# Optimization experiments

Measured on AMD Instinct MI355X. Metric: run time of the kernel, lower is better.

Reference implementation:

```python
import jax, jax.numpy as jnp
import numpy as np

E = 262144      # n_edges
T = 2097152     # n_triplets
F = 128         # embed_size
A = 64          # angle_int_embed_size
RBF = 6         # num_radial
SBF = 42        # num_spherical * num_radial
B = 8           # basis_int_embed_size
NB = 1          # residual layers before skip
NA = 2          # residual layers after skip


def _rn(k, shape):
    # fan-in scaled init like default Linear init
    return jax.random.normal(k, shape, jnp.float32) / np.sqrt(shape[-2])


def setup_inputs() -> dict:
    key = jax.random.key(0)
    ks = jax.random.split(key, 18)
    return dict(
        m_input=jax.random.normal(ks[0], (E, F), jnp.float32),
        rbf=jax.random.normal(ks[1], (E, RBF), jnp.float32),
        sbf=jax.random.normal(ks[2], (T, SBF), jnp.float32),
        reduce_to_ji=jax.random.randint(ks[3], (T,), 0, E),
        expand_to_kj=jax.random.randint(ks[4], (T,), 0, E),
        W_kj=_rn(ks[5], (F, F)), b_kj=jnp.zeros((F,), jnp.float32),
        W_rbf1=_rn(ks[6], (RBF, B)), W_rbf2=_rn(ks[7], (B, F)),
        W_sbf1=_rn(ks[8], (SBF, B)), W_sbf2=_rn(ks[9], (B, A)),
        W_down=_rn(ks[10], (F, A)), W_up=_rn(ks[11], (A, F)),
        W_ji=_rn(ks[12], (F, F)), b_ji=jnp.zeros((F,), jnp.float32),
        W_res_before=_rn(ks[13], (NB, 2, F, F)),
        b_res_before=jnp.zeros((NB, 2, F), jnp.float32),
        W_final=_rn(ks[14], (F, F)), b_final=jnp.zeros((F,), jnp.float32),
        W_res_after=_rn(ks[15], (NA, 2, F, F)),
        b_res_after=jnp.zeros((NA, 2, F), jnp.float32),
    )


def _residual(x, W, b):
    # W: [2, F, F], b: [2, F]; two swish-activated linears + skip
    h = jax.nn.swish(x @ W[0] + b[0])
    h = jax.nn.swish(h @ W[1] + b[1])
    return x + h


def reference(m_input, rbf, sbf, reduce_to_ji, expand_to_kj,
              W_kj, b_kj, W_rbf1, W_rbf2, W_sbf1, W_sbf2,
              W_down, W_up, W_ji, b_ji,
              W_res_before, b_res_before, W_final, b_final,
              W_res_after, b_res_after):
    # dense_kj branch, modulated by projected RBF
    m_ang = jax.nn.swish(m_input @ W_kj + b_kj)          # [E, F]
    rbf_p = (rbf @ W_rbf1) @ W_rbf2                      # [E, F]
    m_ang = m_ang * rbf_p
    m_ang = jax.nn.swish(m_ang @ W_down)                 # [E, A]
    # expand edges -> triplets, modulate with projected SBF
    m_kj = m_ang[expand_to_kj]                           # [T, A]
    sbf_p = (sbf @ W_sbf1) @ W_sbf2                      # [T, A]
    m_kj = m_kj * sbf_p
    # scatter-reduce triplets back to edges (high precision fp32 segment sum)
    agg = jax.ops.segment_sum(m_kj.astype(jnp.float32), reduce_to_ji,
                              num_segments=E)            # [E, A]
    prop = jax.nn.swish(agg @ W_up)                      # [E, F]
    m_ji = jax.nn.swish(m_input @ W_ji + b_ji)           # [E, F]
    m = m_ji + prop
    for i in range(NB):
        m = _residual(m, W_res_before[i], b_res_before[i])
    m = jax.nn.swish(m @ W_final + b_final)
    m = m + m_input
    for i in range(NA):
        m = _residual(m, W_res_after[i], b_res_after[i])
    return m
```

## Files before the change

kernel.cpp:

```cpp
#include <hip/hip_runtime.h>

#define EN 262144
#define TN 2097152
#define CAP 32
#define OFCAP 262144

__device__ __forceinline__ float swishf(float x){ return x/(1.f+__expf(-x)); }

template<int K, int NC, class AF, class EP>
__device__ __forceinline__ void gemm_stage(const float* __restrict__ Wg, AF af, EP ep)
{
  constexpr int CPT = NC/16;
  const int tc = threadIdx.x & 15;
  const int te = threadIdx.x >> 4;
  const int c0 = tc*CPT;
  float acc[4][CPT];
#pragma unroll
  for(int i=0;i<4;i++)
#pragma unroll
    for(int j=0;j<CPT;j++) acc[i][j]=0.f;

  for (int k=0;k<K;k+=4){
    float a[4][4];
#pragma unroll
    for(int i=0;i<4;i++){
      float4 t = af(te*4+i, k);
      a[i][0]=t.x; a[i][1]=t.y; a[i][2]=t.z; a[i][3]=t.w;
    }
#pragma unroll
    for(int kk=0;kk<4;kk++){
      float w[CPT];
      const float* wp = Wg + (size_t)(k+kk)*NC + c0;
      float4 w0 = *(const float4*)wp;
      w[0]=w0.x; w[1]=w0.y; w[2]=w0.z; w[3]=w0.w;
      if constexpr (CPT==8){
        float4 w1 = *(const float4*)(wp+4);
        w[4]=w1.x; w[5]=w1.y; w[6]=w1.z; w[7]=w1.w;
      }
#pragma unroll
      for(int i=0;i<4;i++)
#pragma unroll
        for(int j=0;j<CPT;j++)
          acc[i][j] = fmaf(a[i][kk], w[j], acc[i][j]);
    }
  }
  ep(acc, te, c0);
}

__global__ void k0_prebasis(const float* __restrict__ Ws1, const float* __restrict__ Ws2,
                            const float* __restrict__ Wr1, const float* __restrict__ Wr2,
                            float* __restrict__ Psbf, float* __restrict__ Prbf)
{
  int idx = blockIdx.x*256 + threadIdx.x;
  if (idx < 42*64){
    int r = idx>>6, a = idx&63;
    float s=0.f;
#pragma unroll
    for(int j=0;j<8;j++) s = fmaf(Ws1[r*8+j], Ws2[j*64+a], s);
    Psbf[idx]=s;
  }
  if (idx < 6*128){
    int r = idx>>7, c = idx&127;
    float s=0.f;
#pragma unroll
    for(int j=0;j<8;j++) s = fmaf(Wr1[r*8+j], Wr2[j*128+c], s);
    Prbf[idx]=s;
  }
}

__global__ __launch_bounds__(256) void k1_pre(
  const float* __restrict__ mi, const float* __restrict__ rbf,
  const float* __restrict__ Wkj, const float* __restrict__ bkj,
  const float* __restrict__ Wdown, const float* __restrict__ Prbf,
  float* __restrict__ mang2)
{
  __shared__ __align__(16) float hs[64*128];
  const int eb = blockIdx.x*64;

  auto afG = [&](int e,int k)->float4{
    return *(const float4*)(mi + (size_t)(eb+e)*128 + k);
  };
  gemm_stage<128,128>(Wkj, afG, [&](float (&acc)[4][8], int te, int c0){
    float bb[8];
#pragma unroll
    for(int j=0;j<8;j++) bb[j]=bkj[c0+j];
#pragma unroll
    for(int i=0;i<4;i++){
      int e = te*4+i;
      size_t ge = (size_t)(eb+e);
      float rp[8];
#pragma unroll
      for(int j=0;j<8;j++) rp[j]=0.f;
#pragma unroll
      for(int r=0;r<6;r++){
        float rv = rbf[ge*6+r];
        const float* prow = Prbf + r*128 + c0;
        float4 p0 = *(const float4*)prow;
        float4 p1 = *(const float4*)(prow+4);
        rp[0]=fmaf(rv,p0.x,rp[0]); rp[1]=fmaf(rv,p0.y,rp[1]);
        rp[2]=fmaf(rv,p0.z,rp[2]); rp[3]=fmaf(rv,p0.w,rp[3]);
        rp[4]=fmaf(rv,p1.x,rp[4]); rp[5]=fmaf(rv,p1.y,rp[5]);
        rp[6]=fmaf(rv,p1.z,rp[6]); rp[7]=fmaf(rv,p1.w,rp[7]);
      }
#pragma unroll
      for(int j=0;j<8;j++)
        hs[e*128+c0+j] = swishf(acc[i][j]+bb[j])*rp[j];
    }
  });
  __syncthreads();
  auto afL = [&](int e,int k)->float4{ return *(const float4*)(hs + e*128 + k); };
  gemm_stage<128,64>(Wdown, afL, [&](float (&acc)[4][4], int te, int c0){
#pragma unroll
    for(int i=0;i<4;i++){
      size_t ge = (size_t)(eb + te*4+i);
      float4 v = make_float4(swishf(acc[i][0]),swishf(acc[i][1]),
                             swishf(acc[i][2]),swishf(acc[i][3]));
      *(float4*)(mang2 + ge*64 + c0) = v;
    }
  });
}

__global__ __launch_bounds__(256) void ka_bin(
  const int* __restrict__ rji,
  int* __restrict__ cnt, int* __restrict__ perm,
  int* __restrict__ ofcnt, int* __restrict__ oflist)
{
  size_t t = (size_t)blockIdx.x*256 + threadIdx.x;
  int ji = rji[t];
  int slot = atomicAdd(cnt + ji, 1);
  if (slot < CAP) {
    perm[(size_t)ji*CAP + slot] = (int)t;
  } else {
    int o = atomicAdd(ofcnt, 1);
    if (o < OFCAP) oflist[o] = (int)t;
  }
}

__global__ __launch_bounds__(256) void k2_gather(
  const float* __restrict__ sbf, const int* __restrict__ ekj,
  const int* __restrict__ cnt, const int* __restrict__ perm,
  const float* __restrict__ Psbf, const float* __restrict__ mang2,
  float* __restrict__ agg)
{
  const int lane = threadIdx.x & 63;
  const int wid  = blockIdx.x*4 + (threadIdx.x >> 6);
  const int nw   = gridDim.x*4;

  float P[42];
#pragma unroll
  for (int r=0;r<42;r++) P[r] = Psbf[r*64 + lane];

  for (int e = wid; e < EN; e += nw) {
    int n = cnt[e]; if (n > CAP) n = CAP;
    const int* pl = perm + (size_t)e*CAP;
    float acc = 0.f;
    for (int i=0;i<n;i++) {
      int t  = __builtin_amdgcn_readfirstlane(pl[i]);
      int kj = __builtin_amdgcn_readfirstlane(ekj[t]);
      float mv = mang2[(size_t)kj*64 + lane];
      const float* su = sbf + (size_t)t*42;
      float sp0 = 0.f, sp1 = 0.f;
#pragma unroll
      for (int r=0;r<42;r+=2){
        sp0 = fmaf(su[r],   P[r],   sp0);
        sp1 = fmaf(su[r+1], P[r+1], sp1);
      }
      acc = fmaf(mv, sp0 + sp1, acc);
    }
    agg[(size_t)e*64 + lane] = acc;
  }
}

__global__ __launch_bounds__(256) void kof(
  const int* __restrict__ ofcnt, const int* __restrict__ oflist,
  const float* __restrict__ sbf, const int* __restrict__ rji,
  const int* __restrict__ ekj, const float* __restrict__ Psbf,
  const float* __restrict__ mang2, float* __restrict__ agg)
{
  int n = *ofcnt; if (n > OFCAP) n = OFCAP;
  const int lane = threadIdx.x & 63;
  for (int i = blockIdx.x*4 + (threadIdx.x>>6); i < n; i += gridDim.x*4) {
    int t = oflist[i];
    const float* su = sbf + (size_t)t*42;
    float sp = 0.f;
#pragma unroll
    for (int r=0;r<42;r++) sp = fmaf(su[r], Psbf[r*64+lane], sp);
    float val = mang2[(size_t)ekj[t]*64 + lane] * sp;
    atomicAdd(agg + (size_t)rji[t]*64 + lane, val);
  }
}

__global__ __launch_bounds__(256) void k3_post(
  const float* __restrict__ mi, const float* __restrict__ agg,
  const float* __restrict__ Wup, const float* __restrict__ Wji, const float* __restrict__ bji,
  const float* __restrict__ Wrb, const float* __restrict__ brb,
  const float* __restrict__ Wfin, const float* __restrict__ bfin,
  const float* __restrict__ Wra, const float* __restrict__ bra,
  float* __restrict__ outp)
{
  __shared__ __align__(16) float xs[64*128];
  __shared__ __align__(16) float hs[64*128];
  const int eb = blockIdx.x*64;

  auto afA = [&](int e,int k)->float4{ return *(const float4*)(agg + (size_t)(eb+e)*64 + k); };
  auto afG = [&](int e,int k)->float4{ return *(const float4*)(mi + (size_t)(eb+e)*128 + k); };
  auto afX = [&](int e,int k)->float4{ return *(const float4*)(xs + e*128 + k); };
  auto afH = [&](int e,int k)->float4{ return *(const float4*)(hs + e*128 + k); };

  gemm_stage<64,128>(Wup, afA, [&](float (&acc)[4][8], int te, int c0){
#pragma unroll
    for(int i=0;i<4;i++){ int e=te*4+i;
#pragma unroll
      for(int j=0;j<8;j++) xs[e*128+c0+j] = swishf(acc[i][j]);
    }
  });
  gemm_stage<128,128>(Wji, afG, [&](float (&acc)[4][8], int te, int c0){
    float bb[8];
#pragma unroll
    for(int j=0;j<8;j++) bb[j]=bji[c0+j];
#pragma unroll
    for(int i=0;i<4;i++){ int e=te*4+i;
#pragma unroll
      for(int j=0;j<8;j++) xs[e*128+c0+j] += swishf(acc[i][j]+bb[j]);
    }
  });
  __syncthreads();
  gemm_stage<128,128>(Wrb, afX, [&](float (&acc)[4][8], int te, int c0){
    float bb[8];
#pragma unroll
    for(int j=0;j<8;j++) bb[j]=brb[c0+j];
#pragma unroll
    for(int i=0;i<4;i++){ int e=te*4+i;
#pragma unroll
      for(int j=0;j<8;j++) hs[e*128+c0+j] = swishf(acc[i][j]+bb[j]);
    }
  });
  __syncthreads();
  gemm_stage<128,128>(Wrb+16384, afH, [&](float (&acc)[4][8], int te, int c0){
    float bb[8];
#pragma unroll
    for(int j=0;j<8;j++) bb[j]=brb[128+c0+j];
#pragma unroll
    for(int i=0;i<4;i++){ int e=te*4+i;
#pragma unroll
      for(int j=0;j<8;j++) xs[e*128+c0+j] += swishf(acc[i][j]+bb[j]);
    }
  });
  __syncthreads();
  gemm_stage<128,128>(Wfin, afX, [&](float (&acc)[4][8], int te, int c0){
    float bb[8];
#pragma unroll
    for(int j=0;j<8;j++) bb[j]=bfin[c0+j];
#pragma unroll
    for(int i=0;i<4;i++){ int e=te*4+i;
      const float* p = mi + (size_t)(eb+e)*128 + c0;
      float4 m0 = *(const float4*)p;
      float4 m1 = *(const float4*)(p+4);
      float m[8] = {m0.x,m0.y,m0.z,m0.w,m1.x,m1.y,m1.z,m1.w};
#pragma unroll
      for(int j=0;j<8;j++) hs[e*128+c0+j] = swishf(acc[i][j]+bb[j]) + m[j];
    }
  });
  __syncthreads();
  gemm_stage<128,128>(Wra, afH, [&](float (&acc)[4][8], int te, int c0){
    float bb[8];
#pragma unroll
    for(int j=0;j<8;j++) bb[j]=bra[c0+j];
#pragma unroll
    for(int i=0;i<4;i++){ int e=te*4+i;
#pragma unroll
      for(int j=0;j<8;j++) xs[e*128+c0+j] = swishf(acc[i][j]+bb[j]);
    }
  });
  __syncthreads();
  gemm_stage<128,128>(Wra+16384, afX, [&](float (&acc)[4][8], int te, int c0){
    float bb[8];
#pragma unroll
    for(int j=0;j<8;j++) bb[j]=bra[128+c0+j];
#pragma unroll
    for(int i=0;i<4;i++){ int e=te*4+i;
#pragma unroll
      for(int j=0;j<8;j++) hs[e*128+c0+j] += swishf(acc[i][j]+bb[j]);
    }
  });
  __syncthreads();
  gemm_stage<128,128>(Wra+32768, afH, [&](float (&acc)[4][8], int te, int c0){
    float bb[8];
#pragma unroll
    for(int j=0;j<8;j++) bb[j]=bra[256+c0+j];
#pragma unroll
    for(int i=0;i<4;i++){ int e=te*4+i;
#pragma unroll
      for(int j=0;j<8;j++) xs[e*128+c0+j] = swishf(acc[i][j]+bb[j]);
    }
  });
  __syncthreads();
  gemm_stage<128,128>(Wra+49152, afX, [&](float (&acc)[4][8], int te, int c0){
    float bb[8];
#pragma unroll
    for(int j=0;j<8;j++) bb[j]=bra[384+c0+j];
#pragma unroll
    for(int i=0;i<4;i++){ int e=te*4+i;
      size_t ge = (size_t)(eb+e);
      float o[8];
#pragma unroll
      for(int j=0;j<8;j++) o[j] = hs[e*128+c0+j] + swishf(acc[i][j]+bb[j]);
      *(float4*)(outp + ge*128 + c0)   = make_float4(o[0],o[1],o[2],o[3]);
      *(float4*)(outp + ge*128 + c0+4) = make_float4(o[4],o[5],o[6],o[7]);
    }
  });
}

extern "C" void kernel_launch(void* const* d_in, const int* in_sizes, int n_in,
                              void* d_out, int out_size, void* d_ws, size_t ws_size,
                              hipStream_t stream)
{
  (void)in_sizes; (void)n_in; (void)out_size; (void)ws_size;
  const float* mi   = (const float*)d_in[0];
  const float* rbf  = (const float*)d_in[1];
  const float* sbf  = (const float*)d_in[2];
  const int*   rji  = (const int*)d_in[3];
  const int*   ekj  = (const int*)d_in[4];
  const float* Wkj  = (const float*)d_in[5];
  const float* bkj  = (const float*)d_in[6];
  const float* Wr1  = (const float*)d_in[7];
  const float* Wr2  = (const float*)d_in[8];
  const float* Ws1  = (const float*)d_in[9];
  const float* Ws2  = (const float*)d_in[10];
  const float* Wdn  = (const float*)d_in[11];
  const float* Wup  = (const float*)d_in[12];
  const float* Wji  = (const float*)d_in[13];
  const float* bji  = (const float*)d_in[14];
  const float* Wrb  = (const float*)d_in[15];
  const float* brb  = (const float*)d_in[16];
  const float* Wfin = (const float*)d_in[17];
  const float* bfin = (const float*)d_in[18];
  const float* Wra  = (const float*)d_in[19];
  const float* bra  = (const float*)d_in[20];

  char* ws = (char*)d_ws;
  float* mang2 = (float*)ws;
  float* agg   = (float*)(ws + (size_t)EN*64*4);
  float* Psbf  = (float*)(ws + (size_t)EN*64*8);
  float* Prbf  = Psbf + 42*64;
  int*   cnt   = (int*)(ws + (size_t)EN*64*8 + 65536);
  int*   ofcnt = cnt + EN;
  int*   perm  = (int*)((char*)cnt + (size_t)EN*4 + 256);
  int*   oflist= perm + (size_t)EN*CAP;

  hipMemsetAsync(cnt, 0, (size_t)EN*4 + 256, stream);
  k0_prebasis<<<11, 256, 0, stream>>>(Ws1, Ws2, Wr1, Wr2, Psbf, Prbf);
  ka_bin<<<TN/256, 256, 0, stream>>>(rji, cnt, perm, ofcnt, oflist);
  k1_pre<<<EN/64, 256, 0, stream>>>(mi, rbf, Wkj, bkj, Wdn, Prbf, mang2);
  k2_gather<<<2048, 256, 0, stream>>>(sbf, ekj, cnt, perm, Psbf, mang2, agg);
  kof<<<64, 256, 0, stream>>>(ofcnt, oflist, sbf, rji, ekj, Psbf, mang2, agg);
  k3_post<<<EN/64, 256, 0, stream>>>(mi, agg, Wup, Wji, bji, Wrb, brb,
                                     Wfin, bfin, Wra, bra, (float*)d_out);
}
```

Measured before the change: 2.763 ms.

## Keep residual stream in registers, single padded LDS tile, prefetch gather indices

The post-processing kernel now holds the residual stream (x, h) in registers and uses a single padded LDS buffer (stride 132) for GEMM operand staging. This halves shared memory per block, and launch bounds request 4 blocks per SM for more occupancy. LDS writes are vectorized and padded to reduce bank conflicts in both k1 and k3. The gather kernel loads up to 32 triplet and kj indices per edge in one wave-wide read, broadcasts them with shuffles and prefetches the next mang2 row. The extra syncs and higher register pressure may limit the occupancy gain.

```diff
diff --git a/kernel.cpp b/kernel.cpp
--- a/kernel.cpp
+++ b/kernel.cpp
@@ -4,17 +4,18 @@
 #define TN 2097152
 #define CAP 32
 #define OFCAP 262144
+#define LDP 132
 
 __device__ __forceinline__ float swishf(float x){ return x/(1.f+__expf(-x)); }
 
-template<int K, int NC, class AF, class EP>
-__device__ __forceinline__ void gemm_stage(const float* __restrict__ Wg, AF af, EP ep)
+template<int K, int NC, class AF>
+__device__ __forceinline__ void gemm_core(const float* __restrict__ Wg, AF af,
+                                          float (&acc)[4][NC/16])
 {
   constexpr int CPT = NC/16;
   const int tc = threadIdx.x & 15;
   const int te = threadIdx.x >> 4;
   const int c0 = tc*CPT;
-  float acc[4][CPT];
 #pragma unroll
   for(int i=0;i<4;i++)
 #pragma unroll
@@ -44,7 +45,6 @@
           acc[i][j] = fmaf(a[i][kk], w[j], acc[i][j]);
     }
   }
-  ep(acc, te, c0);
 }
 
 __global__ void k0_prebasis(const float* __restrict__ Ws1, const float* __restrict__ Ws2,
@@ -74,13 +74,18 @@
   const float* __restrict__ Wdown, const float* __restrict__ Prbf,
   float* __restrict__ mang2)
 {
-  __shared__ __align__(16) float hs[64*128];
+  __shared__ __align__(16) float hs[64*LDP];
   const int eb = blockIdx.x*64;
+  const int tc = threadIdx.x & 15;
+  const int te = threadIdx.x >> 4;
 
   auto afG = [&](int e,int k)->float4{
     return *(const float4*)(mi + (size_t)(eb+e)*128 + k);
   };
-  gemm_stage<128,128>(Wkj, afG, [&](float (&acc)[4][8], int te, int c0){
+  float acc[4][8];
+  gemm_core<128,128>(Wkj, afG, acc);
+  {
+    const int c0 = tc*8;
     float bb[8];
 #pragma unroll
     for(int j=0;j<8;j++) bb[j]=bkj[c0+j];
@@ -102,22 +107,28 @@
         rp[4]=fmaf(rv,p1.x,rp[4]); rp[5]=fmaf(rv,p1.y,rp[5]);
         rp[6]=fmaf(rv,p1.z,rp[6]); rp[7]=fmaf(rv,p1.w,rp[7]);
       }
-#pragma unroll
-      for(int j=0;j<8;j++)
-        hs[e*128+c0+j] = swishf(acc[i][j]+bb[j])*rp[j];
-    }
-  });
+      float o[8];
+#pragma unroll
+      for(int j=0;j<8;j++) o[j] = swishf(acc[i][j]+bb[j])*rp[j];
+      float* p = hs + e*LDP + c0;
+      *(float4*)p     = make_float4(o[0],o[1],o[2],o[3]);
+      *(float4*)(p+4) = make_float4(o[4],o[5],o[6],o[7]);
+    }
+  }
   __syncthreads();
-  auto afL = [&](int e,int k)->float4{ return *(const float4*)(hs + e*128 + k); };
-  gemm_stage<128,64>(Wdown, afL, [&](float (&acc)[4][4], int te, int c0){
+  auto afL = [&](int e,int k)->float4{ return *(const float4*)(hs + e*LDP + k); };
+  float acc2[4][4];
+  gemm_core<128,64>(Wdown, afL, acc2);
+  {
+    const int c0 = tc*4;
 #pragma unroll
     for(int i=0;i<4;i++){
       size_t ge = (size_t)(eb + te*4+i);
-      float4 v = make_float4(swishf(acc[i][0]),swishf(acc[i][1]),
-                             swishf(acc[i][2]),swishf(acc[i][3]));
+      float4 v = make_float4(swishf(acc2[i][0]),swishf(acc2[i][1]),
+                             swishf(acc2[i][2]),swishf(acc2[i][3]));
       *(float4*)(mang2 + ge*64 + c0) = v;
     }
-  });
+  }
 }
 
 __global__ __launch_bounds__(256) void ka_bin(
@@ -153,19 +164,32 @@
   for (int e = wid; e < EN; e += nw) {
     int n = cnt[e]; if (n > CAP) n = CAP;
     const int* pl = perm + (size_t)e*CAP;
+    int tv  = (lane < n) ? pl[lane] : 0;
+    int kjv = (lane < n) ? ekj[tv]  : 0;
+
     float acc = 0.f;
+    int tcur = 0; float mvcur = 0.f;
+    if (n > 0) {
+      tcur = __builtin_amdgcn_readfirstlane(__shfl(tv, 0));
+      int kj0 = __builtin_amdgcn_readfirstlane(__shfl(kjv, 0));
+      mvcur = mang2[(size_t)kj0*64 + lane];
+    }
     for (int i=0;i<n;i++) {
-      int t  = __builtin_amdgcn_readfirstlane(pl[i]);
-      int kj = __builtin_amdgcn_readfirstlane(ekj[t]);
-      float mv = mang2[(size_t)kj*64 + lane];
-      const float* su = sbf + (size_t)t*42;
+      int tnext = 0; float mvnext = 0.f;
+      if (i+1 < n) {
+        tnext = __builtin_amdgcn_readfirstlane(__shfl(tv, i+1));
+        int kjn = __builtin_amdgcn_readfirstlane(__shfl(kjv, i+1));
+        mvnext = mang2[(size_t)kjn*64 + lane];
+      }
+      const float* su = sbf + (size_t)tcur*42;
       float sp0 = 0.f, sp1 = 0.f;
 #pragma unroll
       for (int r=0;r<42;r+=2){
         sp0 = fmaf(su[r],   P[r],   sp0);
         sp1 = fmaf(su[r+1], P[r+1], sp1);
       }
-      acc = fmaf(mv, sp0 + sp1, acc);
+      acc = fmaf(mvcur, sp0 + sp1, acc);
+      tcur = tnext; mvcur = mvnext;
     }
     agg[(size_t)e*64 + lane] = acc;
   }
@@ -190,7 +214,7 @@
   }
 }
 
-__global__ __launch_bounds__(256) void k3_post(
+__global__ __launch_bounds__(256, 4) void k3_post(
   const float* __restrict__ mi, const float* __restrict__ agg,
   const float* __restrict__ Wup, const float* __restrict__ Wji, const float* __restrict__ bji,
   const float* __restrict__ Wrb, const float* __restrict__ brb,
@@ -198,117 +222,123 @@
   const float* __restrict__ Wra, const float* __restrict__ bra,
   float* __restrict__ outp)
 {
-  __shared__ __align__(16) float xs[64*128];
-  __shared__ __align__(16) float hs[64*128];
+  __shared__ __align__(16) float Ls[64*LDP];
   const int eb = blockIdx.x*64;
+  const int tc = threadIdx.x & 15;
+  const int te = threadIdx.x >> 4;
+  const int c0 = tc*8;
 
   auto afA = [&](int e,int k)->float4{ return *(const float4*)(agg + (size_t)(eb+e)*64 + k); };
   auto afG = [&](int e,int k)->float4{ return *(const float4*)(mi + (size_t)(eb+e)*128 + k); };
-  auto afX = [&](int e,int k)->float4{ return *(const float4*)(xs + e*128 + k); };
-  auto afH = [&](int e,int k)->float4{ return *(const float4*)(hs + e*128 + k); };
-
-  gemm_stage<64,128>(Wup, afA, [&](float (&acc)[4][8], int te, int c0){
-#pragma unroll
-    for(int i=0;i<4;i++){ int e=te*4+i;
-#pragma unroll
-      for(int j=0;j<8;j++) xs[e*128+c0+j] = swishf(acc[i][j]);
-    }
-  });
-  gemm_stage<128,128>(Wji, afG, [&](float (&acc)[4][8], int te, int c0){
+  auto afL = [&](int e,int k)->float4{ return *(const float4*)(Ls + e*LDP + k); };
+
+  auto WR = [&](float (&v)[4][8]){
+#pragma unroll
+    for(int i=0;i<4;i++){
+      float* p = Ls + (te*4+i)*LDP + c0;
+      *(float4*)p     = make_float4(v[i][0],v[i][1],v[i][2],v[i][3]);
+      *(float4*)(p+4) = make_float4(v[i][4],v[i][5],v[i][6],v[i][7]);
+    }
+  };
+  auto WRS = [&](float (&a)[4][8], const float* __restrict__ b){
+    float bb[8];
+#pragma unroll
+    for(int j=0;j<8;j++) bb[j]=b[c0+j];
+#pragma unroll
+    for(int i=0;i<4;i++){
+      float* p = Ls + (te*4+i)*LDP + c0;
+      *(float4*)p     = make_float4(swishf(a[i][0]+bb[0]),swishf(a[i][1]+bb[1]),
+                                    swishf(a[i][2]+bb[2]),swishf(a[i][3]+bb[3]));
+      *(float4*)(p+4) = make_float4(swishf(a[i][4]+bb[4]),swishf(a[i][5]+bb[5]),
+                                    swishf(a[i][6]+bb[6]),swishf(a[i][7]+bb[7]));
+    }
+  };
+
+  float x[4][8], h[4][8], acc[4][8];
+
+  gemm_core<64,128>(Wup, afA, acc);
+#pragma unroll
+  for(int i=0;i<4;i++)
+#pragma unroll
+    for(int j=0;j<8;j++) x[i][j] = swishf(acc[i][j]);
+
+  gemm_core<128,128>(Wji, afG, acc);
+  {
     float bb[8];
 #pragma unroll
     for(int j=0;j<8;j++) bb[j]=bji[c0+j];
 #pragma unroll
-    for(int i=0;i<4;i++){ int e=te*4+i;
-#pragma unroll
-      for(int j=0;j<8;j++) xs[e*128+c0+j] += swishf(acc[i][j]+bb[j]);
-    }
-  });
-  __syncthreads();
-  gemm_stage<128,128>(Wrb, afX, [&](float (&acc)[4][8], int te, int c0){
-    float bb[8];
-#pragma unroll
-    for(int j=0;j<8;j++) bb[j]=brb[c0+j];
-#pragma unroll
-    for(int i=0;i<4;i++){ int e=te*4+i;
-#pragma unroll
-      for(int j=0;j<8;j++) hs[e*128+c0+j] = swishf(acc[i][j]+bb[j]);
-    }
-  });
-  __syncthreads();
-  gemm_stage<128,128>(Wrb+16384, afH, [&](float (&acc)[4][8], int te, int c0){
+    for(int i=0;i<4;i++)
+#pragma unroll
+      for(int j=0;j<8;j++) x[i][j] += swishf(acc[i][j]+bb[j]);
+  }
+  WR(x); __syncthreads();
+
+  gemm_core<128,128>(Wrb, afL, acc);
+  __syncthreads(); WRS(acc, brb); __syncthreads();
+
+  gemm_core<128,128>(Wrb+16384, afL, acc);
+  {
     float bb[8];
 #pragma unroll
     for(int j=0;j<8;j++) bb[j]=brb[128+c0+j];
 #pragma unroll
-    for(int i=0;i<4;i++){ int e=te*4+i;
-#pragma unroll
-      for(int j=0;j<8;j++) xs[e*128+c0+j] += swishf(acc[i][j]+bb[j]);
-    }
-  });
-  __syncthreads();
-  gemm_stage<128,128>(Wfin, afX, [&](float (&acc)[4][8], int te, int c0){
+    for(int i=0;i<4;i++)
+#pragma unroll
+      for(int j=0;j<8;j++) x[i][j] += swishf(acc[i][j]+bb[j]);
+  }
+  __syncthreads(); WR(x); __syncthreads();
+
+  gemm_core<128,128>(Wfin, afL, acc);
+  {
     float bb[8];
 #pragma unroll
     for(int j=0;j<8;j++) bb[j]=bfin[c0+j];
 #pragma unroll
-    for(int i=0;i<4;i++){ int e=te*4+i;
-      const float* p = mi + (size_t)(eb+e)*128 + c0;
+    for(int i=0;i<4;i++){
+      const float* p = mi + (size_t)(eb+te*4+i)*128 + c0;
       float4 m0 = *(const float4*)p;
       float4 m1 = *(const float4*)(p+4);
       float m[8] = {m0.x,m0.y,m0.z,m0.w,m1.x,m1.y,m1.z,m1.w};
 #pragma unroll
-      for(int j=0;j<8;j++) hs[e*128+c0+j] = swishf(acc[i][j]+bb[j]) + m[j];
-    }
-  });
-  __syncthreads();
-  gemm_stage<128,128>(Wra, afH, [&](float (&acc)[4][8], int te, int c0){
-    float bb[8];
-#pragma unroll
-    for(int j=0;j<8;j++) bb[j]=bra[c0+j];
-#pragma unroll
-    for(int i=0;i<4;i++){ int e=te*4+i;
-#pragma unroll
-      for(int j=0;j<8;j++) xs[e*128+c0+j] = swishf(acc[i][j]+bb[j]);
-    }
-  });
-  __syncthreads();
-  gemm_stage<128,128>(Wra+16384, afX, [&](float (&acc)[4][8], int te, int c0){
+      for(int j=0;j<8;j++) h[i][j] = swishf(acc[i][j]+bb[j]) + m[j];
+    }
+  }
+  __syncthreads(); WR(h); __syncthreads();
+
+  gemm_core<128,128>(Wra, afL, acc);
+  __syncthreads(); WRS(acc, bra); __syncthreads();
+
+  gemm_core<128,128>(Wra+16384, afL, acc);
+  {
     float bb[8];
 #pragma unroll
     for(int j=0;j<8;j++) bb[j]=bra[128+c0+j];
 #pragma unroll
-    for(int i=0;i<4;i++){ int e=te*4+i;
-#pragma unroll
-      for(int j=0;j<8;j++) hs[e*128+c0+j] += swishf(acc[i][j]+bb[j]);
-    }
-  });
-  __syncthreads();
-  gemm_stage<128,128>(Wra+32768, afH, [&](float (&acc)[4][8], int te, int c0){
-    float bb[8];
-#pragma unroll
-    for(int j=0;j<8;j++) bb[j]=bra[256+c0+j];
-#pragma unroll
-    for(int i=0;i<4;i++){ int e=te*4+i;
-#pragma unroll
-      for(int j=0;j<8;j++) xs[e*128+c0+j] = swishf(acc[i][j]+bb[j]);
-    }
-  });
-  __syncthreads();
-  gemm_stage<128,128>(Wra+49152, afX, [&](float (&acc)[4][8], int te, int c0){
+    for(int i=0;i<4;i++)
+#pragma unroll
+      for(int j=0;j<8;j++) h[i][j] += swishf(acc[i][j]+bb[j]);
+  }
+  __syncthreads(); WR(h); __syncthreads();
+
+  gemm_core<128,128>(Wra+32768, afL, acc);
+  __syncthreads(); WRS(acc, bra+256); __syncthreads();
+
+  gemm_core<128,128>(Wra+49152, afL, acc);
+  {
     float bb[8];
 #pragma unroll
     for(int j=0;j<8;j++) bb[j]=bra[384+c0+j];
 #pragma unroll
-    for(int i=0;i<4;i++){ int e=te*4+i;
-      size_t ge = (size_t)(eb+e);
+    for(int i=0;i<4;i++){
+      size_t ge = (size_t)(eb+te*4+i);
       float o[8];
 #pragma unroll
-      for(int j=0;j<8;j++) o[j] = hs[e*128+c0+j] + swishf(acc[i][j]+bb[j]);
+      for(int j=0;j<8;j++) o[j] = h[i][j] + swishf(acc[i][j]+bb[j]);
       *(float4*)(outp + ge*128 + c0)   = make_float4(o[0],o[1],o[2],o[3]);
       *(float4*)(outp + ge*128 + c0+4) = make_float4(o[4],o[5],o[6],o[7]);
     }
-  });
+  }
 }
 
 extern "C" void kernel_launch(void* const* d_in, const int* in_sizes, int n_in,
```

After: 3.156 ms. 14.2% more time.
